# Optimization experiments

Measured on AMD Instinct MI355X. Metric: run time of the kernel, lower is better.

## Reference

```python
import jax, jax.numpy as jnp
import numpy as np

_JPEG_QUANT_TABLE = np.array([
    [16, 11, 10, 16, 24, 40, 51, 61],
    [12, 12, 14, 19, 26, 58, 60, 55],
    [14, 13, 16, 24, 40, 57, 69, 56],
    [14, 17, 22, 29, 51, 87, 80, 62],
    [18, 22, 37, 56, 68, 109, 103, 77],
    [24, 35, 55, 64, 81, 104, 113, 92],
    [49, 64, 78, 87, 103, 121, 120, 101],
    [72, 92, 95, 98, 112, 100, 103, 99]], dtype=np.float32)


def _dct_matrix():
    # Orthonormal 8x8 DCT-II basis: D[k, i] = alpha(k) * cos(pi*(2i+1)k/16)
    n = 8
    k = np.arange(n)[:, None].astype(np.float64)
    i = np.arange(n)[None, :].astype(np.float64)
    alpha = np.where(k == 0, np.sqrt(1.0 / n), np.sqrt(2.0 / n))
    return jnp.asarray(alpha * np.cos(np.pi * (2 * i + 1) * k / (2 * n)), dtype=jnp.float32)


def setup_inputs() -> dict:
    key = jax.random.key(0)
    image = jax.random.uniform(key, (32, 3, 512, 512), dtype=jnp.float32)
    return {"image": image, "quality": 75}


def reference(image, quality):
    B, C, H, W = image.shape  # H, W divisible by 8 (no padding branch needed)
    bh, bw = H // 8, W // 8

    # libjpeg quality -> scale (quality is a static Python int)
    scale = 5000.0 / quality if quality < 50 else 200.0 - 2.0 * quality
    qtable = jnp.clip(jnp.asarray(_JPEG_QUANT_TABLE) * scale / 100.0, 1.0, 255.0)
    dct = _dct_matrix()

    x = image - 0.5
    # blockify: (B,C,H,W) -> (B*C, bh, bw, 8, 8)
    blocks = x.reshape(B * C, bh, 8, bw, 8).transpose(0, 1, 3, 2, 4)

    # 2D DCT: dct @ block @ dct^T
    dct_blocks = jnp.einsum('ki,...ij,lj->...kl', dct, blocks, dct)

    # quantize with straight-through estimator (forward: round, backward: identity)
    normalized = dct_blocks / qtable
    quantized = normalized + jax.lax.stop_gradient(jnp.round(normalized) - normalized)
    dequantized = quantized * qtable

    # 2D IDCT: dct^T @ block @ dct
    spatial = jnp.einsum('ki,...kl,lj->...ij', dct, dequantized, dct)

    # deblockify: (B*C, bh, bw, 8, 8) -> (B, C, H, W)
    result = spatial.transpose(0, 1, 3, 2, 4).reshape(B, C, H, W)
    return jnp.clip(result + 0.5, 0.0, 1.0)
```

## Files before the change

kernel.cpp:

```cpp
#include <hip/hip_runtime.h>


typedef float v4f __attribute__((ext_vector_type(4)));

static __device__ __constant__ float c_qbase[64] = {
    16.f, 11.f, 10.f, 16.f, 24.f, 40.f, 51.f, 61.f,
    12.f, 12.f, 14.f, 19.f, 26.f, 58.f, 60.f, 55.f,
    14.f, 13.f, 16.f, 24.f, 40.f, 57.f, 69.f, 56.f,
    14.f, 17.f, 22.f, 29.f, 51.f, 87.f, 80.f, 62.f,
    18.f, 22.f, 37.f, 56.f, 68.f, 109.f, 103.f, 77.f,
    24.f, 35.f, 55.f, 64.f, 81.f, 104.f, 113.f, 92.f,
    49.f, 64.f, 78.f, 87.f, 103.f, 121.f, 120.f, 101.f,
    72.f, 92.f, 95.f, 98.f, 112.f, 100.f, 103.f, 99.f
};

#define LDS_PITCH 9

__global__ __launch_bounds__(256, 8)
void jpeg_row_kernel(const float* __restrict__ in, const int* __restrict__ qual,
                     float* __restrict__ out) {
    constexpr float D[8][8] = {
        { 0.3535533906f,  0.3535533906f,  0.3535533906f,  0.3535533906f,
          0.3535533906f,  0.3535533906f,  0.3535533906f,  0.3535533906f },
        { 0.4903926402f,  0.4157348062f,  0.2777851165f,  0.0975451610f,
         -0.0975451610f, -0.2777851165f, -0.4157348062f, -0.4903926402f },
        { 0.4619397663f,  0.1913417162f, -0.1913417162f, -0.4619397663f,
         -0.4619397663f, -0.1913417162f,  0.1913417162f,  0.4619397663f },
        { 0.4157348062f, -0.0975451610f, -0.4903926402f, -0.2777851165f,
          0.2777851165f,  0.4903926402f,  0.0975451610f, -0.4157348062f },
        { 0.3535533906f, -0.3535533906f, -0.3535533906f,  0.3535533906f,
          0.3535533906f, -0.3535533906f, -0.3535533906f,  0.3535533906f },
        { 0.2777851165f, -0.4903926402f,  0.0975451610f,  0.4157348062f,
         -0.4157348062f, -0.0975451610f,  0.4903926402f, -0.2777851165f },
        { 0.1913417162f, -0.4619397663f,  0.4619397663f, -0.1913417162f,
         -0.1913417162f,  0.4619397663f, -0.4619397663f,  0.1913417162f },
        { 0.0975451610f, -0.2777851165f,  0.4157348062f, -0.4903926402f,
          0.4903926402f, -0.4157348062f,  0.2777851165f, -0.0975451610f }
    };

    __shared__ float qlds[64];
    __shared__ float tr[256 * LDS_PITCH];

    const int tid = threadIdx.x;

    {
        int q = qual[0];
        double sd = (q < 50) ? (5000.0 / (double)q) : (200.0 - 2.0 * (double)q);
        float scale = (float)sd;
        int e = tid & 63;
        float v = c_qbase[e] * scale / 100.0f;
        qlds[e] = fminf(fmaxf(v, 1.0f), 255.0f);
    }

    const int gt  = blockIdx.x * 256 + tid;
    const int b   = gt >> 3;
    const int r   = gt & 7;
    const int img = b >> 12;
    const int by  = (b >> 6) & 63;
    const int bx  = b & 63;
    const long rowaddr = (((long)img * 512 + (long)by * 8 + r) * 512) + (long)bx * 8;

    float x[8];
    {
        const float4 a  = *reinterpret_cast<const float4*>(in + rowaddr);
        const float4 b4 = *reinterpret_cast<const float4*>(in + rowaddr + 4);
        x[0] = a.x - 0.5f; x[1] = a.y - 0.5f; x[2] = a.z - 0.5f; x[3] = a.w - 0.5f;
        x[4] = b4.x - 0.5f; x[5] = b4.y - 0.5f; x[6] = b4.z - 0.5f; x[7] = b4.w - 0.5f;
    }

    float qc[8];
#pragma unroll
    for (int k = 0; k < 8; ++k) qc[k] = qlds[k * 8 + r];

    float u[8];
#pragma unroll
    for (int l = 0; l < 8; ++l) {
        float s = 0.0f;
#pragma unroll
        for (int j = 0; j < 8; ++j) s = fmaf(x[j], D[l][j], s);
        u[l] = s;
    }

    const int base_w = tid * LDS_PITCH;
    const int base_r = (tid & ~7) * LDS_PITCH;
#pragma unroll
    for (int j = 0; j < 8; ++j) tr[base_w + j] = u[j];
    float t[8];
#pragma unroll
    for (int j = 0; j < 8; ++j) t[j] = tr[base_r + j * LDS_PITCH + r];

    float y[8];
#pragma unroll
    for (int k = 0; k < 8; ++k) {
        float s = 0.0f;
#pragma unroll
        for (int j = 0; j < 8; ++j) s = fmaf(D[k][j], t[j], s);
        y[k] = rintf(s / qc[k]) * qc[k];
    }

    float v[8];
#pragma unroll
    for (int j = 0; j < 8; ++j) {
        float s = 0.0f;
#pragma unroll
        for (int k = 0; k < 8; ++k) s = fmaf(D[k][j], y[k], s);
        v[j] = s;
    }

#pragma unroll
    for (int j = 0; j < 8; ++j) tr[base_w + j] = v[j];
    float w[8];
#pragma unroll
    for (int j = 0; j < 8; ++j) w[j] = tr[base_r + j * LDS_PITCH + r];

    float srow[8];
#pragma unroll
    for (int c = 0; c < 8; ++c) {
        float s = 0.0f;
#pragma unroll
        for (int l = 0; l < 8; ++l) s = fmaf(w[l], D[l][c], s);
        s += 0.5f;
        srow[c] = fminf(fmaxf(s, 0.0f), 1.0f);
    }
    v4f o0 = { srow[0], srow[1], srow[2], srow[3] };
    v4f o1 = { srow[4], srow[5], srow[6], srow[7] };
    __builtin_nontemporal_store(o0, reinterpret_cast<v4f*>(out + rowaddr));
    __builtin_nontemporal_store(o1, reinterpret_cast<v4f*>(out + rowaddr + 4));
}

extern "C" void kernel_launch(void* const* d_in, const int* in_sizes, int n_in,
                              void* d_out, int out_size, void* d_ws, size_t ws_size,
                              hipStream_t stream) {
    const float* img  = (const float*)d_in[0];
    const int*   qual = (const int*)d_in[1];
    float*       out  = (float*)d_out;

    const int nthreads_total = (out_size / 64) * 8;
    const int block = 256;
    const int grid = nthreads_total / block;

    jpeg_row_kernel<<<grid, block, 0, stream>>>(img, qual, out);
}
```

Before: 43.95 us.

## Use even/odd DCT butterfly decomposition and reciprocal quantization

```diff
diff --git a/kernel.cpp b/kernel.cpp
--- a/kernel.cpp
+++ b/kernel.cpp
@@ -19,26 +19,20 @@
 __global__ __launch_bounds__(256, 8)
 void jpeg_row_kernel(const float* __restrict__ in, const int* __restrict__ qual,
                      float* __restrict__ out) {
-    constexpr float D[8][8] = {
-        { 0.3535533906f,  0.3535533906f,  0.3535533906f,  0.3535533906f,
-          0.3535533906f,  0.3535533906f,  0.3535533906f,  0.3535533906f },
-        { 0.4903926402f,  0.4157348062f,  0.2777851165f,  0.0975451610f,
-         -0.0975451610f, -0.2777851165f, -0.4157348062f, -0.4903926402f },
-        { 0.4619397663f,  0.1913417162f, -0.1913417162f, -0.4619397663f,
-         -0.4619397663f, -0.1913417162f,  0.1913417162f,  0.4619397663f },
-        { 0.4157348062f, -0.0975451610f, -0.4903926402f, -0.2777851165f,
-          0.2777851165f,  0.4903926402f,  0.0975451610f, -0.4157348062f },
-        { 0.3535533906f, -0.3535533906f, -0.3535533906f,  0.3535533906f,
-          0.3535533906f, -0.3535533906f, -0.3535533906f,  0.3535533906f },
-        { 0.2777851165f, -0.4903926402f,  0.0975451610f,  0.4157348062f,
-         -0.4157348062f, -0.0975451610f,  0.4903926402f, -0.2777851165f },
-        { 0.1913417162f, -0.4619397663f,  0.4619397663f, -0.1913417162f,
-         -0.1913417162f,  0.4619397663f, -0.4619397663f,  0.1913417162f },
-        { 0.0975451610f, -0.2777851165f,  0.4157348062f, -0.4903926402f,
-          0.4903926402f, -0.4157348062f,  0.2777851165f, -0.0975451610f }
+    constexpr float CE[4][4] = {
+        { 0.3535533906f,  0.3535533906f,  0.3535533906f,  0.3535533906f },
+        { 0.4619397663f,  0.1913417162f, -0.1913417162f, -0.4619397663f },
+        { 0.3535533906f, -0.3535533906f, -0.3535533906f,  0.3535533906f },
+        { 0.1913417162f, -0.4619397663f,  0.4619397663f, -0.1913417162f }
+    };
+    constexpr float CO[4][4] = {
+        { 0.4903926402f,  0.4157348062f,  0.2777851165f,  0.0975451610f },
+        { 0.4157348062f, -0.0975451610f, -0.4903926402f, -0.2777851165f },
+        { 0.2777851165f, -0.4903926402f,  0.0975451610f,  0.4157348062f },
+        { 0.0975451610f, -0.2777851165f,  0.4157348062f, -0.4903926402f }
     };
 
-    __shared__ float qlds[64];
+    __shared__ float2 qlds[64];
     __shared__ float tr[256 * LDS_PITCH];
 
     const int tid = threadIdx.x;
@@ -49,7 +43,8 @@
         float scale = (float)sd;
         int e = tid & 63;
         float v = c_qbase[e] * scale / 100.0f;
-        qlds[e] = fminf(fmaxf(v, 1.0f), 255.0f);
+        v = fminf(fmaxf(v, 1.0f), 255.0f);
+        qlds[e] = make_float2(v, 1.0f / v);
     }
 
     const int gt  = blockIdx.x * 256 + tid;
@@ -68,17 +63,28 @@
         x[4] = b4.x - 0.5f; x[5] = b4.y - 0.5f; x[6] = b4.z - 0.5f; x[7] = b4.w - 0.5f;
     }
 
-    float qc[8];
+    float qk[8], rqk[8];
 #pragma unroll
-    for (int k = 0; k < 8; ++k) qc[k] = qlds[k * 8 + r];
+    for (int k = 0; k < 8; ++k) {
+        float2 t2 = qlds[k * 8 + r];
+        qk[k] = t2.x; rqk[k] = t2.y;
+    }
 
     float u[8];
+    {
+        float e[4], o[4];
 #pragma unroll
-    for (int l = 0; l < 8; ++l) {
-        float s = 0.0f;
+        for (int j = 0; j < 4; ++j) { e[j] = x[j] + x[7 - j]; o[j] = x[j] - x[7 - j]; }
 #pragma unroll
-        for (int j = 0; j < 8; ++j) s = fmaf(x[j], D[l][j], s);
-        u[l] = s;
+        for (int m = 0; m < 4; ++m) {
+            float se = 0.0f, so = 0.0f;
+#pragma unroll
+            for (int j = 0; j < 4; ++j) {
+                se = fmaf(e[j], CE[m][j], se);
+                so = fmaf(o[j], CO[m][j], so);
+            }
+            u[2 * m] = se; u[2 * m + 1] = so;
+        }
     }
 
     const int base_w = tid * LDS_PITCH;
@@ -90,21 +96,33 @@
     for (int j = 0; j < 8; ++j) t[j] = tr[base_r + j * LDS_PITCH + r];
 
     float y[8];
+    {
+        float e[4], o[4];
 #pragma unroll
-    for (int k = 0; k < 8; ++k) {
-        float s = 0.0f;
+        for (int j = 0; j < 4; ++j) { e[j] = t[j] + t[7 - j]; o[j] = t[j] - t[7 - j]; }
 #pragma unroll
-        for (int j = 0; j < 8; ++j) s = fmaf(D[k][j], t[j], s);
-        y[k] = rintf(s / qc[k]) * qc[k];
+        for (int m = 0; m < 4; ++m) {
+            float se = 0.0f, so = 0.0f;
+#pragma unroll
+            for (int j = 0; j < 4; ++j) {
+                se = fmaf(e[j], CE[m][j], se);
+                so = fmaf(o[j], CO[m][j], so);
+            }
+            y[2 * m]     = rintf(se * rqk[2 * m])     * qk[2 * m];
+            y[2 * m + 1] = rintf(so * rqk[2 * m + 1]) * qk[2 * m + 1];
+        }
     }
 
     float v[8];
 #pragma unroll
-    for (int j = 0; j < 8; ++j) {
-        float s = 0.0f;
+    for (int j = 0; j < 4; ++j) {
+        float a = 0.0f, bb = 0.0f;
 #pragma unroll
-        for (int k = 0; k < 8; ++k) s = fmaf(D[k][j], y[k], s);
-        v[j] = s;
+        for (int m = 0; m < 4; ++m) {
+            a  = fmaf(y[2 * m],     CE[m][j], a);
+            bb = fmaf(y[2 * m + 1], CO[m][j], bb);
+        }
+        v[j] = a + bb; v[7 - j] = a - bb;
     }
 
 #pragma unroll
@@ -115,17 +133,20 @@
 
     float srow[8];
 #pragma unroll
-    for (int c = 0; c < 8; ++c) {
-        float s = 0.0f;
+    for (int j = 0; j < 4; ++j) {
+        float a = 0.0f, bb = 0.0f;
 #pragma unroll
-        for (int l = 0; l < 8; ++l) s = fmaf(w[l], D[l][c], s);
-        s += 0.5f;
-        srow[c] = fminf(fmaxf(s, 0.0f), 1.0f);
+        for (int m = 0; m < 4; ++m) {
+            a  = fmaf(w[2 * m],     CE[m][j], a);
+            bb = fmaf(w[2 * m + 1], CO[m][j], bb);
+        }
+        float s0 = a + bb + 0.5f;
+        float s1 = a - bb + 0.5f;
+        srow[j]     = fminf(fmaxf(s0, 0.0f), 1.0f);
+        srow[7 - j] = fminf(fmaxf(s1, 0.0f), 1.0f);
     }
-    v4f o0 = { srow[0], srow[1], srow[2], srow[3] };
-    v4f o1 = { srow[4], srow[5], srow[6], srow[7] };
-    __builtin_nontemporal_store(o0, reinterpret_cast<v4f*>(out + rowaddr));
-    __builtin_nontemporal_store(o1, reinterpret_cast<v4f*>(out + rowaddr + 4));
+    *reinterpret_cast<float4*>(out + rowaddr)     = make_float4(srow[0], srow[1], srow[2], srow[3]);
+    *reinterpret_cast<float4*>(out + rowaddr + 4) = make_float4(srow[4], srow[5], srow[6], srow[7]);
 }
 
 extern "C" void kernel_launch(void* const* d_in, const int* in_sizes, int n_in,
```

Result: faster. 38.69 us (-12.0%).
